# Kernel tuning notes

Hardware: AMD Instinct MI355X
Metric: run time of the kernel (lower is better)

Reference implementation:

```python
import jax, jax.numpy as jnp
import numpy as np

NUM_HEADS = 16
THETA = 10000.0


def _rope(x, pos, theta):
    # x: [B, H, S, D], pos: [S] ints. Interleaved-pair RoPE.
    D = x.shape[-1]
    half = D // 2
    inv_freq = theta ** (-(jnp.arange(half, dtype=jnp.float32) * 2.0) / D)  # [half]
    ang = pos.astype(jnp.float32)[:, None] * inv_freq[None, :]              # [S, half]
    cos, sin = jnp.cos(ang), jnp.sin(ang)
    x1 = x[..., 0::2]
    x2 = x[..., 1::2]
    r1 = x1 * cos - x2 * sin
    r2 = x1 * sin + x2 * cos
    return jnp.stack([r1, r2], axis=-1).reshape(x.shape)


def setup_inputs() -> dict:
    key = jax.random.key(0)
    ks = jax.random.split(key, 5)
    B, S, D = 4, 2048, 1024
    scale = 1.0 / np.sqrt(D)
    x = jax.random.normal(ks[0], (B, S, D), dtype=jnp.float32)
    Wq = jax.random.normal(ks[1], (D, D), dtype=jnp.float32) * scale
    Wk = jax.random.normal(ks[2], (D, D), dtype=jnp.float32) * scale
    Wv = jax.random.normal(ks[3], (D, D), dtype=jnp.float32) * scale
    Wo = jax.random.normal(ks[4], (D, D), dtype=jnp.float32) * scale
    token_positions = jnp.arange(S, dtype=jnp.int64)
    return {"x": x, "Wq": Wq, "Wk": Wk, "Wv": Wv, "Wo": Wo,
            "token_positions": token_positions}


def reference(x, Wq, Wk, Wv, Wo, token_positions):
    B, S, D = x.shape
    H = NUM_HEADS
    hd = D // H
    # Projections (weights stored as [d_model, d_k], matching the transposed params)
    q = jnp.einsum('bsd,de->bse', x, Wq).reshape(B, S, H, hd).transpose(0, 2, 1, 3)
    k = jnp.einsum('bsd,de->bse', x, Wk).reshape(B, S, H, hd).transpose(0, 2, 1, 3)
    v = jnp.einsum('bsd,de->bse', x, Wv).reshape(B, S, H, hd).transpose(0, 2, 1, 3)
    # RoPE on q and k
    q = _rope(q, token_positions, THETA)
    k = _rope(k, token_positions, THETA)
    # Causal scaled dot-product attention
    scores = jnp.einsum('bhqd,bhkd->bhqk', q, k) / jnp.sqrt(jnp.float32(hd))
    causal = jnp.tril(jnp.ones((S, S), dtype=bool))
    scores = jnp.where(causal, scores, jnp.float32(-jnp.inf))
    attn = jax.nn.softmax(scores, axis=-1)
    o = jnp.einsum('bhqk,bhkd->bhqd', attn, v)          # [B, H, S, hd]
    o = o.transpose(0, 2, 1, 3).reshape(B, S, D)         # [B, S, D]
    return jnp.einsum('bsd,de->bse', o, Wo)
```

## Files before the change

### kernel.cpp

```cpp
#include <hip/hip_runtime.h>
#include <math.h>

#define B_ 4
#define S_ 2048
#define D_ 1024
#define H_ 16
#define HD_ 64
#define ES_F 0.180336880111f
#define KF (-0.41524101186f)

typedef unsigned short ushort_t;
typedef __attribute__((ext_vector_type(8))) short short8;
typedef __attribute__((ext_vector_type(4))) short short4_t;
typedef __attribute__((ext_vector_type(4))) float f32x4;
typedef __attribute__((ext_vector_type(16))) float f32x16;
typedef __attribute__((ext_vector_type(2))) unsigned uint2v;

typedef const void __attribute__((address_space(1))) gvoid;
typedef void __attribute__((address_space(3))) lvoid;

__device__ __forceinline__ ushort_t f2bf(float f) {
    union { float f; unsigned u; } v; v.f = f;
    unsigned r = (v.u + 0x7FFFu + ((v.u >> 16) & 1u)) >> 16;
    return (ushort_t)r;
}
__device__ __forceinline__ float fexp2(float x) {
#if __has_builtin(__builtin_amdgcn_exp2f)
    return __builtin_amdgcn_exp2f(x);
#else
    return exp2f(x);
#endif
}
__device__ __forceinline__ unsigned pk2t(float a, float b) {
    union { float f; unsigned u; } A, Bv; A.f = a; Bv.f = b;
#if __has_builtin(__builtin_amdgcn_perm)
    return __builtin_amdgcn_perm(Bv.u, A.u, 0x07060302u);
#else
    return (A.u >> 16) | (Bv.u & 0xFFFF0000u);
#endif
}
__device__ __forceinline__ short8 mk_frag(unsigned a, unsigned b, unsigned c, unsigned d) {
    union { unsigned u[4]; short8 s; } t;
    t.u[0] = a; t.u[1] = b; t.u[2] = c; t.u[3] = d; return t.s;
}

__global__ __launch_bounds__(256)
void cvt_x(const float* __restrict__ x, ushort_t* __restrict__ xb)
{
    const size_t i = ((size_t)blockIdx.x * 256 + threadIdx.x) * 8;
    float4 a = *(const float4*)&x[i];
    float4 b = *(const float4*)&x[i + 4];
    short8 o;
    o[0] = (short)f2bf(a.x); o[1] = (short)f2bf(a.y);
    o[2] = (short)f2bf(a.z); o[3] = (short)f2bf(a.w);
    o[4] = (short)f2bf(b.x); o[5] = (short)f2bf(b.y);
    o[6] = (short)f2bf(b.z); o[7] = (short)f2bf(b.w);
    *(short8*)&xb[i] = o;
}

__global__ __launch_bounds__(256)
void cvt_wt4(const float* __restrict__ W0, const float* __restrict__ W1,
             const float* __restrict__ W2, const float* __restrict__ W3,
             ushort_t* __restrict__ T0, ushort_t* __restrict__ T1,
             ushort_t* __restrict__ T2, ushort_t* __restrict__ T3)
{
    const int z = blockIdx.z;
    const float* W = (z == 0) ? W0 : (z == 1) ? W1 : (z == 2) ? W2 : W3;
    ushort_t* Wt = (z == 0) ? T0 : (z == 1) ? T1 : (z == 2) ? T2 : T3;

    __shared__ __align__(16) float T[64 * 68];
    const int t = threadIdx.x;
    const int k0 = blockIdx.y * 64, n0 = blockIdx.x * 64;
    const int row = t >> 2, c0 = (t & 3) * 16;
#pragma unroll
    for (int u = 0; u < 4; ++u)
        *(float4*)&T[row * 68 + c0 + u * 4] =
            *(const float4*)&W[(size_t)(k0 + row) * D_ + n0 + c0 + u * 4];
    __syncthreads();
    const int n = t >> 2, kc = (t & 3) * 16;
    short8 o0, o1;
#pragma unroll
    for (int kk = 0; kk < 8; ++kk) o0[kk] = (short)f2bf(T[(kc + kk) * 68 + n]);
#pragma unroll
    for (int kk = 0; kk < 8; ++kk) o1[kk] = (short)f2bf(T[(kc + 8 + kk) * 68 + n]);
    *(short8*)&Wt[(size_t)(n0 + n) * D_ + k0 + kc] = o0;
    *(short8*)&Wt[(size_t)(n0 + n) * D_ + k0 + kc + 8] = o1;
}


#define STAGE(tt, Ad, Bd) {                                                    \
    const int kk_ = (tt) * 64;                                                 \
    _Pragma("unroll") for (int i_ = 0; i_ < 4; ++i_) {                         \
        const int rb_ = (i_ * 4 + w) * 8;                                      \
        __builtin_amdgcn_global_load_lds(                                      \
            (gvoid*)&pA[(size_t)(aBase + rb_ + srow) * D_ + kk_ + sch],        \
            (lvoid*)&(Ad)[rb_ * 64], 16, 0, 0);                                \
        __builtin_amdgcn_global_load_lds(                                      \
            (gvoid*)&pB[(size_t)(bBase + rb_ + srow) * D_ + kk_ + sch],        \
            (lvoid*)&(Bd)[rb_ * 64], 16, 0, 0);                                \
    } }

#define COMPUTE(Ab, Bb) {                                                      \
    _Pragma("unroll") for (int ks = 0; ks < 4; ++ks) {                         \
        const int xr_ = (((ks * 2 + hl) ^ (lq & 7)) << 3);                     \
        short8 af0 = *(const short8*)&(Ab)[(wr * 64 + lq) * 64 + xr_];         \
        short8 af1 = *(const short8*)&(Ab)[(wr * 64 + 32 + lq) * 64 + xr_];    \
        short8 bf0 = *(const short8*)&(Bb)[(wc * 64 + lq) * 64 + xr_];         \
        short8 bf1 = *(const short8*)&(Bb)[(wc * 64 + 32 + lq) * 64 + xr_];    \
        acc[0][0] = __builtin_amdgcn_mfma_f32_32x32x16_bf16(af0, bf0, acc[0][0], 0, 0, 0); \
        acc[0][1] = __builtin_amdgcn_mfma_f32_32x32x16_bf16(af0, bf1, acc[0][1], 0, 0, 0); \
        acc[1][0] = __builtin_amdgcn_mfma_f32_32x32x16_bf16(af1, bf0, acc[1][0], 0, 0, 0); \
        acc[1][1] = __builtin_amdgcn_mfma_f32_32x32x16_bf16(af1, bf1, acc[1][1], 0, 0, 0); \
    } }

__global__ __launch_bounds__(256, 2)
void gemm_bt(const ushort_t* __restrict__ A,
             const ushort_t* __restrict__ W0, const ushort_t* __restrict__ W1,
             const ushort_t* __restrict__ W2,
             void* __restrict__ d0, void* __restrict__ d1, void* __restrict__ d2,
             const int mode_base)
{
    __shared__ __align__(16) ushort_t As[2 * 128 * 64];
    __shared__ __align__(16) ushort_t Bs[2 * 128 * 64];

    const int tid = threadIdx.x;
    const int lane = tid & 63;
    const int hl = lane >> 5;
    const int lq = lane & 31;
    const int w = tid >> 6, wr = w >> 1, wc = w & 1;
    const int z = blockIdx.z;
    const ushort_t* Wt = (z == 0) ? W0 : (z == 1) ? W1 : W2;
    const int mode = mode_base + z;
    const bool sw = (mode == 0) || (mode == 1);

    const int tokT = blockIdx.x * 128, featT = blockIdx.y * 128;
    const ushort_t* pA = sw ? Wt : A;
    const ushort_t* pB = sw ? A : Wt;
    const int aBase = sw ? featT : tokT;
    const int bBase = sw ? tokT : featT;

    const f32x16 zv16 = {0,0,0,0,0,0,0,0,0,0,0,0,0,0,0,0};
    f32x16 acc[2][2];
    acc[0][0] = zv16; acc[0][1] = zv16; acc[1][0] = zv16; acc[1][1] = zv16;

    const int srow = lane >> 3;
    const int spc  = lane & 7;
    const int sch  = (spc ^ srow) * 8;

    ushort_t* A0 = As;  ushort_t* A1 = As + 128 * 64;
    ushort_t* B0 = Bs;  ushort_t* B1 = Bs + 128 * 64;

    STAGE(0, A0, B0);
    __syncthreads();

#pragma unroll 1
    for (int t2 = 0; t2 < 8; ++t2) {
        STAGE(2 * t2 + 1, A1, B1);
        COMPUTE(A0, B0);
        __syncthreads();
        if (t2 < 7) STAGE(2 * t2 + 2, A0, B0);
        COMPUTE(A1, B1);
        __syncthreads();
    }

    if (mode == 2) {
#pragma unroll
        for (int tn = 0; tn < 2; ++tn) {
            const int n = bBase + wc * 64 + tn * 32 + lq;
            const int h = n >> 6, dd = n & 63;
#pragma unroll
            for (int tm = 0; tm < 2; ++tm) {
                const int mb = aBase + wr * 64 + tm * 32 + 4 * hl;
#pragma unroll
                for (int g = 0; g < 4; ++g) {
                    const int m_base = mb + 8 * g;
                    const int bb2 = m_base >> 11, s0 = m_base & (S_ - 1);
                    short4_t pk;
#pragma unroll
                    for (int r = 0; r < 4; ++r)
                        pk[r] = (short)f2bf(acc[tm][tn][4 * g + r]);
                    *(short4_t*)&((ushort_t*)d2)[(((size_t)bb2 * H_ + h) * HD_ + dd) * S_ + s0] = pk;
                }
            }
        }
    } else if (mode == 3) {
        float* outp = (float*)d0;
#pragma unroll
        for (int tn = 0; tn < 2; ++tn) {
            const int n = bBase + wc * 64 + tn * 32 + lq;
#pragma unroll
            for (int tm = 0; tm < 2; ++tm) {
                const int mb = aBase + wr * 64 + tm * 32 + 4 * hl;
#pragma unroll
                for (int g = 0; g < 4; ++g)
#pragma unroll
                    for (int r = 0; r < 4; ++r)
                        outp[(size_t)(mb + 8 * g + r) * D_ + n] =
                            acc[tm][tn][4 * g + r];
            }
        }
    } else {
        ushort_t* dst = (mode == 0) ? (ushort_t*)d0 : (ushort_t*)d1;
        const float sc = (mode == 0) ? ES_F : 1.0f;
#pragma unroll
        for (int tn = 0; tn < 2; ++tn) {
            const int tok = bBase + wc * 64 + tn * 32 + lq;
            const int bb2 = tok >> 11, s0 = tok & (S_ - 1);
            const float fs0 = (float)s0;
#pragma unroll
            for (int tm = 0; tm < 2; ++tm) {
                const int fb = aBase + wr * 64 + tm * 32 + 4 * hl;
                const int h = fb >> 6;
                const int ddb = fb & 63;
                ushort_t* dp = &dst[(((size_t)bb2 * H_ + h) * S_ + s0) * HD_];
#pragma unroll
                for (int g = 0; g < 4; ++g) {
                    const int dd = ddb + 8 * g;
                    const int jj = dd >> 1;
                    const float if0 = exp2f(KF * (float)jj);
                    const float if1 = exp2f(KF * (float)(jj + 1));
                    float sn0, cs0, sn1, cs1;
                    __sincosf(fs0 * if0, &sn0, &cs0);
                    __sincosf(fs0 * if1, &sn1, &cs1);
                    const float x0 = acc[tm][tn][4 * g + 0];
                    const float x1 = acc[tm][tn][4 * g + 1];
                    const float x2 = acc[tm][tn][4 * g + 2];
                    const float x3 = acc[tm][tn][4 * g + 3];
                    short4_t pk;
                    pk[0] = (short)f2bf((x0 * cs0 - x1 * sn0) * sc);
                    pk[1] = (short)f2bf((x0 * sn0 + x1 * cs0) * sc);
                    pk[2] = (short)f2bf((x2 * cs1 - x3 * sn1) * sc);
                    pk[3] = (short)f2bf((x2 * sn1 + x3 * cs1) * sc);
                    *(short4_t*)&dp[dd] = pk;
                }
            }
        }
    }
}

__global__ __launch_bounds__(256)
void attn_mfma(const ushort_t* __restrict__ Q, const ushort_t* __restrict__ K,
               const ushort_t* __restrict__ Vt, ushort_t* __restrict__ O)
{
    __shared__ __align__(16) ushort_t sK[64 * 64];
    __shared__ __align__(16) ushort_t sVt[64 * 64];

    const int tid = threadIdx.x;
    const int lane = tid & 63;
    const int hl = lane >> 5;
    const int lq = lane & 31;
    const int w = tid >> 6;
    const int hb64 = blockIdx.x;
    const int pair = blockIdx.y;
    const int h = hb64 >> 2, bb = hb64 & 3;
    const size_t hb = ((size_t)(bb * H_ + h)) * S_ * HD_;

    const int srow = lane >> 3;
    const int spc = lane & 7;

    short8 ones;
#pragma unroll
    for (int i = 0; i < 8; ++i) ones[i] = (short)0x3F80;

    const f32x16 zv16 = {0,0,0,0,0,0,0,0,0,0,0,0,0,0,0,0};

    for (int pass = 0; pass < 2; ++pass) {
        const int q0 = ((pass == 0) ? (15 - pair) : pair) * 128;
        const int wq = q0 + w * 32;
        const int qg = wq + lq;

        short8 qf[4];
#pragma unroll
        for (int ks = 0; ks < 4; ++ks)
            qf[ks] = *(const short8*)&Q[hb + (size_t)qg * HD_ + ks * 16 + hl * 8];

        f32x16 oa[2], la;
        oa[0] = zv16; oa[1] = zv16; la = zv16;

        const int nt = q0 / 64 + 2;
        for (int kt = 0; kt < nt; ++kt) {
            const int k0 = kt * 64;
            __syncthreads();
            {
#pragma unroll
                for (int i = 0; i < 2; ++i) {
                    const int row = i * 32 + w * 8 + srow;
                    const int sc = (spc ^ (row & 7)) * 8;
                    __builtin_amdgcn_global_load_lds(
                        (gvoid*)&K[hb + (size_t)(k0 + row) * HD_ + sc],
                        (lvoid*)&sK[(i * 32 + w * 8) * 64], 16, 0, 0);
                    __builtin_amdgcn_global_load_lds(
                        (gvoid*)&Vt[hb + (size_t)row * S_ + k0 + sc],
                        (lvoid*)&sVt[(i * 32 + w * 8) * 64], 16, 0, 0);
                }
            }
            __syncthreads();

            if (k0 > wq + 31) continue;

            f32x16 st[2];
            st[0] = zv16; st[1] = zv16;
            const int kr0 = lq, kr1 = 32 + lq;
#pragma unroll
            for (int ks = 0; ks < 4; ++ks) {
                const int ch = ks * 2 + hl;
                short8 ak0 = *(const short8*)&sK[kr0 * 64 + ((ch ^ (kr0 & 7)) << 3)];
                short8 ak1 = *(const short8*)&sK[kr1 * 64 + ((ch ^ (kr1 & 7)) << 3)];
                st[0] = __builtin_amdgcn_mfma_f32_32x32x16_bf16(ak0, qf[ks], st[0], 0, 0, 0);
                st[1] = __builtin_amdgcn_mfma_f32_32x32x16_bf16(ak1, qf[ks], st[1], 0, 0, 0);
            }

            const bool diag = (k0 + 63 > wq);
            short8 pf[4];
#pragma unroll
            for (int nt2 = 0; nt2 < 2; ++nt2) {
                float pv[16];
                const int kb = k0 + nt2 * 32 + 4 * hl;
#pragma unroll
                for (int g = 0; g < 4; ++g)
#pragma unroll
                    for (int r = 0; r < 4; ++r) {
                        float s = st[nt2][4 * g + r];
                        if (diag) {
                            const int key = kb + 8 * g + r;
                            s = (key <= qg) ? s : -INFINITY;
                        }
                        pv[4 * g + r] = fexp2(s);
                    }
                unsigned P2[8];
#pragma unroll
                for (int g = 0; g < 4; ++g) {
                    P2[2 * g]     = pk2t(pv[4 * g + 0], pv[4 * g + 1]);
                    P2[2 * g + 1] = pk2t(pv[4 * g + 2], pv[4 * g + 3]);
                }
#if __has_builtin(__builtin_amdgcn_permlane32_swap)
                uint2v r02 = __builtin_amdgcn_permlane32_swap(P2[0], P2[2], false, false);
                uint2v r13 = __builtin_amdgcn_permlane32_swap(P2[1], P2[3], false, false);
                uint2v r46 = __builtin_amdgcn_permlane32_swap(P2[4], P2[6], false, false);
                uint2v r57 = __builtin_amdgcn_permlane32_swap(P2[5], P2[7], false, false);
                pf[nt2 * 2 + 0] = mk_frag(r02[0], r13[0], r02[1], r13[1]);
                pf[nt2 * 2 + 1] = mk_frag(r46[0], r57[0], r46[1], r57[1]);
#else
                unsigned X[8];
#pragma unroll
                for (int m = 0; m < 8; ++m) X[m] = (unsigned)__shfl_xor((int)P2[m], 32);
                pf[nt2 * 2 + 0] = hl ? mk_frag(X[2], X[3], P2[2], P2[3])
                                     : mk_frag(P2[0], P2[1], X[0], X[1]);
                pf[nt2 * 2 + 1] = hl ? mk_frag(X[6], X[7], P2[6], P2[7])
                                     : mk_frag(P2[4], P2[5], X[4], X[5]);
#endif
            }

            const int vr0 = lq, vr1 = 32 + lq;
#pragma unroll
            for (int ks2 = 0; ks2 < 4; ++ks2) {
                const int ch = ks2 * 2 + hl;
                short8 av0 = *(const short8*)&sVt[vr0 * 64 + ((ch ^ (vr0 & 7)) << 3)];
                short8 av1 = *(const short8*)&sVt[vr1 * 64 + ((ch ^ (vr1 & 7)) << 3)];
                oa[0] = __builtin_amdgcn_mfma_f32_32x32x16_bf16(av0, pf[ks2], oa[0], 0, 0, 0);
                oa[1] = __builtin_amdgcn_mfma_f32_32x32x16_bf16(av1, pf[ks2], oa[1], 0, 0, 0);
                la    = __builtin_amdgcn_mfma_f32_32x32x16_bf16(ones, pf[ks2], la, 0, 0, 0);
            }
        }

        const float inv = 1.f / la[0];
        ushort_t* Ob = &O[((size_t)(bb * S_ + qg)) * D_ + h * HD_];
#pragma unroll
        for (int mt = 0; mt < 2; ++mt)
#pragma unroll
            for (int g = 0; g < 4; ++g) {
                short4_t pk;
#pragma unroll
                for (int r = 0; r < 4; ++r)
                    pk[r] = (short)f2bf(oa[mt][4 * g + r] * inv);
                *(short4_t*)&Ob[mt * 32 + 8 * g + 4 * hl] = pk;
            }
    }
}

extern "C" void kernel_launch(void* const* d_in, const int* in_sizes, int n_in,
                              void* d_out, int out_size, void* d_ws, size_t ws_size,
                              hipStream_t stream)
{
    (void)in_sizes; (void)n_in; (void)out_size; (void)ws_size;
    const float* x  = (const float*)d_in[0];
    const float* Wq = (const float*)d_in[1];
    const float* Wk = (const float*)d_in[2];
    const float* Wv = (const float*)d_in[3];
    const float* Wo = (const float*)d_in[4];

    float* out = (float*)d_out;
    ushort_t* ws = (ushort_t*)d_ws;
    const size_t NX = (size_t)B_ * S_ * D_;
    const size_t NW = (size_t)D_ * D_;
    ushort_t* xb  = ws;
    ushort_t* Wqt = xb + NX;
    ushort_t* Wkt = Wqt + NW;
    ushort_t* Wvt = Wkt + NW;
    ushort_t* Wot = Wvt + NW;
    ushort_t* Qb  = Wot + NW;
    ushort_t* Kb  = Qb + NX;
    ushort_t* Vtb = Kb + NX;
    ushort_t* Ob  = Vtb + NX;

    cvt_x<<<dim3(NX / 2048), 256, 0, stream>>>(x, xb);
    cvt_wt4<<<dim3(16, 16, 4), 256, 0, stream>>>(Wq, Wk, Wv, Wo, Wqt, Wkt, Wvt, Wot);

    gemm_bt<<<dim3(64, 8, 3), 256, 0, stream>>>(xb, Wqt, Wkt, Wvt, Qb, Kb, Vtb, 0);
    attn_mfma<<<dim3(64, 8), 256, 0, stream>>>(Qb, Kb, Vtb, Ob);
    gemm_bt<<<dim3(64, 8, 1), 256, 0, stream>>>(Ob, Wot, Wot, Wot, out, nullptr, nullptr, 3);
}
```

Measured before the change: 255.5 us.

## Triple-buffer GEMM with K=32 stages and compute softmax row sums in registers

The projection GEMM moves from double-buffered 64-wide K tiles to a three-stage ring of 32-wide tiles. It uses explicit vmcnt waits and a single barrier per step so two loads stay in flight during compute, and the occupancy hint rises to 3 blocks per CU. The attention kernel drops the extra MFMA that multiplied P by a ones vector to get the softmax denominator and instead sums the fp32 probabilities per lane, combining halves with a cross-lane shuffle. The new denominator sums the unrounded fp32 values rather than the bf16-rounded ones used in P·V, which slightly changes normalization numerics.

Result: slower. 265.5 us (+3.9%).

```diff
diff --git a/kernel.cpp b/kernel.cpp
--- a/kernel.cpp
+++ b/kernel.cpp
@@ -88,40 +88,42 @@
 }
 
 
-#define STAGE(tt, Ad, Bd) {                                                    \
-    const int kk_ = (tt) * 64;                                                 \
-    _Pragma("unroll") for (int i_ = 0; i_ < 4; ++i_) {                         \
-        const int rb_ = (i_ * 4 + w) * 8;                                      \
+#define BSZ_ (128 * 32)
+
+#define STAGE32(tt, off) {                                                     \
+    const int kk_ = (tt) * 32;                                                 \
+    _Pragma("unroll") for (int i_ = 0; i_ < 2; ++i_) {                         \
+        const int rb_ = w * 32 + i_ * 16;                                      \
         __builtin_amdgcn_global_load_lds(                                      \
             (gvoid*)&pA[(size_t)(aBase + rb_ + srow) * D_ + kk_ + sch],        \
-            (lvoid*)&(Ad)[rb_ * 64], 16, 0, 0);                                \
+            (lvoid*)&As[(off) + rb_ * 32], 16, 0, 0);                          \
         __builtin_amdgcn_global_load_lds(                                      \
             (gvoid*)&pB[(size_t)(bBase + rb_ + srow) * D_ + kk_ + sch],        \
-            (lvoid*)&(Bd)[rb_ * 64], 16, 0, 0);                                \
+            (lvoid*)&Bs[(off) + rb_ * 32], 16, 0, 0);                          \
     } }
 
-#define COMPUTE(Ab, Bb) {                                                      \
-    _Pragma("unroll") for (int ks = 0; ks < 4; ++ks) {                         \
-        const int xr_ = (((ks * 2 + hl) ^ (lq & 7)) << 3);                     \
-        short8 af0 = *(const short8*)&(Ab)[(wr * 64 + lq) * 64 + xr_];         \
-        short8 af1 = *(const short8*)&(Ab)[(wr * 64 + 32 + lq) * 64 + xr_];    \
-        short8 bf0 = *(const short8*)&(Bb)[(wc * 64 + lq) * 64 + xr_];         \
-        short8 bf1 = *(const short8*)&(Bb)[(wc * 64 + 32 + lq) * 64 + xr_];    \
+#define COMPUTE32(off) {                                                       \
+    _Pragma("unroll") for (int ks = 0; ks < 2; ++ks) {                         \
+        const int xr_ = (((ks * 2 + hl) ^ (lq & 3)) << 3);                     \
+        short8 af0 = *(const short8*)&As[(off) + (wr * 64 + lq) * 32 + xr_];   \
+        short8 af1 = *(const short8*)&As[(off) + (wr * 64 + 32 + lq) * 32 + xr_]; \
+        short8 bf0 = *(const short8*)&Bs[(off) + (wc * 64 + lq) * 32 + xr_];   \
+        short8 bf1 = *(const short8*)&Bs[(off) + (wc * 64 + 32 + lq) * 32 + xr_]; \
         acc[0][0] = __builtin_amdgcn_mfma_f32_32x32x16_bf16(af0, bf0, acc[0][0], 0, 0, 0); \
         acc[0][1] = __builtin_amdgcn_mfma_f32_32x32x16_bf16(af0, bf1, acc[0][1], 0, 0, 0); \
         acc[1][0] = __builtin_amdgcn_mfma_f32_32x32x16_bf16(af1, bf0, acc[1][0], 0, 0, 0); \
         acc[1][1] = __builtin_amdgcn_mfma_f32_32x32x16_bf16(af1, bf1, acc[1][1], 0, 0, 0); \
     } }
 
-__global__ __launch_bounds__(256, 2)
+__global__ __launch_bounds__(256, 3)
 void gemm_bt(const ushort_t* __restrict__ A,
              const ushort_t* __restrict__ W0, const ushort_t* __restrict__ W1,
              const ushort_t* __restrict__ W2,
              void* __restrict__ d0, void* __restrict__ d1, void* __restrict__ d2,
              const int mode_base)
 {
-    __shared__ __align__(16) ushort_t As[2 * 128 * 64];
-    __shared__ __align__(16) ushort_t Bs[2 * 128 * 64];
+    __shared__ __align__(16) ushort_t As[3 * BSZ_];
+    __shared__ __align__(16) ushort_t Bs[3 * BSZ_];
 
     const int tid = threadIdx.x;
     const int lane = tid & 63;
@@ -143,24 +145,30 @@
     f32x16 acc[2][2];
     acc[0][0] = zv16; acc[0][1] = zv16; acc[1][0] = zv16; acc[1][1] = zv16;
 
-    const int srow = lane >> 3;
-    const int spc  = lane & 7;
-    const int sch  = (spc ^ srow) * 8;
-
-    ushort_t* A0 = As;  ushort_t* A1 = As + 128 * 64;
-    ushort_t* B0 = Bs;  ushort_t* B1 = Bs + 128 * 64;
-
-    STAGE(0, A0, B0);
-    __syncthreads();
+    const int srow = lane >> 2;
+    const int spc  = lane & 3;
+    const int sch  = (spc ^ (srow & 3)) * 8;
+
+    int o0 = 0, o1 = BSZ_, o2 = 2 * BSZ_;
+
+    STAGE32(0, o0);
+    STAGE32(1, o1);
+    __builtin_amdgcn_sched_barrier(0);
+    asm volatile("s_waitcnt vmcnt(4)" ::: "memory");
+    __builtin_amdgcn_s_barrier();
 
 #pragma unroll 1
-    for (int t2 = 0; t2 < 8; ++t2) {
-        STAGE(2 * t2 + 1, A1, B1);
-        COMPUTE(A0, B0);
-        __syncthreads();
-        if (t2 < 7) STAGE(2 * t2 + 2, A0, B0);
-        COMPUTE(A1, B1);
-        __syncthreads();
+    for (int t = 0; t < 32; ++t) {
+        if (t + 2 < 32) STAGE32(t + 2, o2);
+        COMPUTE32(o0);
+        __builtin_amdgcn_sched_barrier(0);
+        if (t + 2 < 32) {
+            asm volatile("s_waitcnt vmcnt(4)" ::: "memory");
+        } else {
+            asm volatile("s_waitcnt vmcnt(0)" ::: "memory");
+        }
+        __builtin_amdgcn_s_barrier();
+        const int tmp = o0; o0 = o1; o1 = o2; o2 = tmp;
     }
 
     if (mode == 2) {
@@ -258,10 +266,6 @@
     const int srow = lane >> 3;
     const int spc = lane & 7;
 
-    short8 ones;
-#pragma unroll
-    for (int i = 0; i < 8; ++i) ones[i] = (short)0x3F80;
-
     const f32x16 zv16 = {0,0,0,0,0,0,0,0,0,0,0,0,0,0,0,0};
 
     for (int pass = 0; pass < 2; ++pass) {
@@ -274,8 +278,9 @@
         for (int ks = 0; ks < 4; ++ks)
             qf[ks] = *(const short8*)&Q[hb + (size_t)qg * HD_ + ks * 16 + hl * 8];
 
-        f32x16 oa[2], la;
-        oa[0] = zv16; oa[1] = zv16; la = zv16;
+        f32x16 oa[2];
+        oa[0] = zv16; oa[1] = zv16;
+        float ls = 0.f;
 
         const int nt = q0 / 64 + 2;
         for (int kt = 0; kt < nt; ++kt) {
@@ -327,6 +332,8 @@
                         }
                         pv[4 * g + r] = fexp2(s);
                     }
+#pragma unroll
+                for (int m = 0; m < 16; ++m) ls += pv[m];
                 unsigned P2[8];
 #pragma unroll
                 for (int g = 0; g < 4; ++g) {
@@ -359,11 +366,11 @@
                 short8 av1 = *(const short8*)&sVt[vr1 * 64 + ((ch ^ (vr1 & 7)) << 3)];
                 oa[0] = __builtin_amdgcn_mfma_f32_32x32x16_bf16(av0, pf[ks2], oa[0], 0, 0, 0);
                 oa[1] = __builtin_amdgcn_mfma_f32_32x32x16_bf16(av1, pf[ks2], oa[1], 0, 0, 0);
-                la    = __builtin_amdgcn_mfma_f32_32x32x16_bf16(ones, pf[ks2], la, 0, 0, 0);
             }
         }
 
-        const float inv = 1.f / la[0];
+        const float lsum = ls + __shfl_xor(ls, 32);
+        const float inv = 1.f / lsum;
         ushort_t* Ob = &O[((size_t)(bb * S_ + qg)) * D_ + h * HD_];
 #pragma unroll
         for (int mt = 0; mt < 2; ++mt)
```
